# Kernel optimization log

Hardware: AMD Instinct MI355X
Metric: run time of the kernel (lower is better)

The kernel has to match this reference:

```python
import jax, jax.numpy as jnp
import numpy as np

EMBED = 2048
HEADS = 16
DFF = 4 * EMBED
EPS = 1e-5


def layernorm(x, g, b):
    mu = jnp.mean(x, axis=-1, keepdims=True)
    var = jnp.var(x, axis=-1, keepdims=True)
    return (x - mu) * jax.lax.rsqrt(var + EPS) * g + b


def setup_inputs() -> dict:
    key = jax.random.key(0)
    ks = jax.random.split(key, 16)
    s = 1.0 / np.sqrt(EMBED)
    sf = 1.0 / np.sqrt(DFF)
    return {
        "x": jax.random.normal(ks[0], (2, 2048, EMBED), jnp.float32),
        "Wq": jax.random.normal(ks[1], (EMBED, EMBED), jnp.float32) * s,
        "bq": jnp.zeros((EMBED,), jnp.float32),
        "Wk": jax.random.normal(ks[2], (EMBED, EMBED), jnp.float32) * s,
        "bk": jnp.zeros((EMBED,), jnp.float32),
        "Wv": jax.random.normal(ks[3], (EMBED, EMBED), jnp.float32) * s,
        "bv": jnp.zeros((EMBED,), jnp.float32),
        "Wo": jax.random.normal(ks[4], (EMBED, EMBED), jnp.float32) * s,
        "bo": jnp.zeros((EMBED,), jnp.float32),
        "g1": jnp.ones((EMBED,), jnp.float32),
        "b1": jnp.zeros((EMBED,), jnp.float32),
        "g2": jnp.ones((EMBED,), jnp.float32),
        "b2": jnp.zeros((EMBED,), jnp.float32),
        "W1": jax.random.normal(ks[5], (EMBED, DFF), jnp.float32) * s,
        "bf1": jnp.zeros((DFF,), jnp.float32),
        "W2": jax.random.normal(ks[6], (DFF, EMBED), jnp.float32) * sf,
        "bf2": jnp.zeros((EMBED,), jnp.float32),
    }


def reference(x, Wq, bq, Wk, bk, Wv, bv, Wo, bo, g1, b1, g2, b2, W1, bf1, W2, bf2):
    B, N, C = x.shape
    H = HEADS
    hd = C // H
    # QKV projections -> [B, H, N, hd]
    def split_heads(t):
        return t.reshape(B, N, H, hd).transpose(0, 2, 1, 3)
    q = split_heads(x @ Wq + bq)
    k = split_heads(x @ Wk + bk)
    v = split_heads(x @ Wv + bv)
    # scores [B, H, N, N]
    attn = jnp.einsum('bhqd,bhkd->bhqk', q, k) / np.sqrt(hd)
    attn = jax.nn.softmax(attn, axis=-1)
    out = jnp.einsum('bhqk,bhkd->bhqd', attn, v)
    out = out.transpose(0, 2, 1, 3).reshape(B, N, C)
    out = out @ Wo + bo
    h = layernorm(x + out, g1, b1)
    ff = jax.nn.gelu(h @ W1 + bf1, approximate=False) @ W2 + bf2
    return layernorm(h + ff, g2, b2)
```

## Files before the change

kernel.cpp:

```cpp
#include <hip/hip_runtime.h>
#include <math.h>

#define EMBED 2048
#define DFF   8192
#define TOK   4096
#define SEQ   2048
#define HEADS 16
#define HD    128
#define LDQ   6144

typedef __attribute__((ext_vector_type(8))) short short8;
typedef __attribute__((ext_vector_type(4))) float f32x4;

__device__ __forceinline__ unsigned short f2bf(float f) {
    unsigned int u = __float_as_uint(f);
    return (unsigned short)((u + 0x7FFFu + ((u >> 16) & 1u)) >> 16);
}
__device__ __forceinline__ float bf2f(unsigned short s) {
    return __uint_as_float(((unsigned int)s) << 16);
}

__device__ __forceinline__ void async16(const void* g, void* l) {
    __builtin_amdgcn_global_load_lds((const __attribute__((address_space(1))) void*)g,
                                     (__attribute__((address_space(3))) void*)l, 16, 0, 0);
}

__device__ __forceinline__ float gelu_fast(float v) {
    const float y = 1.5957691216057308f * (v + 0.044715f * v * v * v);
    return v / (1.0f + __expf(-y));
}

template<int MODE>
__global__ __launch_bounds__(256, 2)
void gemm_bf16(const unsigned short* __restrict__ A, const unsigned short* __restrict__ B,
               const float* __restrict__ bias, const void* __restrict__ resid,
               unsigned short* __restrict__ C, int M, int N, int K, int lda)
{
    __shared__ __align__(16) float smemf[8448];
    unsigned short* As = (unsigned short*)smemf;
    unsigned short* Bs = As + 8192;
    float* Cs = smemf;

    const int t = threadIdx.x;
    const int w = t >> 6, l = t & 63;
    const int quad = l >> 4, m16 = l & 15;
    const long bm = (long)blockIdx.y * 128, bn = (long)blockIdx.x * 128;
    const int wr = (w >> 1)*64, wc = (w & 1)*64;

    f32x4 acc[4][4] = {};

    const int srow = w*16 + (l >> 2);
    const int sslot = l & 3;
    const unsigned short* Ag = A + (size_t)bm*lda;
    const unsigned short* Bg = B + (size_t)bn*K;

#pragma unroll
    for (int u = 0; u < 2; ++u) {
        const int row = u*64 + srow;
        const int c = sslot ^ ((row >> 1) & 3);
        async16(Ag + (size_t)row*lda + c*8, &As[u*2048 + w*512]);
        async16(Bg + (size_t)row*K   + c*8, &Bs[u*2048 + w*512]);
    }

    const int iters = K >> 5;
    for (int it = 0; it < iters; ++it) {
        __syncthreads();
        if (it + 1 < iters) {
            const int k0 = (it + 1) << 5;
            const int bo = ((it + 1) & 1) * 4096;
#pragma unroll
            for (int u = 0; u < 2; ++u) {
                const int row = u*64 + srow;
                const int c = sslot ^ ((row >> 1) & 3);
                async16(Ag + (size_t)row*lda + k0 + c*8, &As[bo + u*2048 + w*512]);
                async16(Bg + (size_t)row*K   + k0 + c*8, &Bs[bo + u*2048 + w*512]);
            }
        }
        const int co = (it & 1) * 4096;
        short8 af[4], bf[4];
#pragma unroll
        for (int s = 0; s < 4; ++s) {
            const int ra = wr + s*16 + m16;
            const int sla = quad ^ ((ra >> 1) & 3);
            af[s] = *(const short8*)&As[co + ra*32 + sla*8];
            const int rb = wc + s*16 + m16;
            const int slb = quad ^ ((rb >> 1) & 3);
            bf[s] = *(const short8*)&Bs[co + rb*32 + slb*8];
        }
#pragma unroll
        for (int ms = 0; ms < 4; ++ms)
#pragma unroll
            for (int ns = 0; ns < 4; ++ns)
                acc[ms][ns] = __builtin_amdgcn_mfma_f32_16x16x32_bf16(af[ms], bf[ns], acc[ms][ns], 0, 0, 0);
    }

    const int ecol = (t & 15) * 8;
    float bias8[8];
#pragma unroll
    for (int i = 0; i < 8; ++i) bias8[i] = bias[bn + ecol + i];

#pragma unroll
    for (int pass = 0; pass < 2; ++pass) {
        __syncthreads();
        if ((w >> 1) == pass) {
#pragma unroll
            for (int ms = 0; ms < 4; ++ms)
#pragma unroll
                for (int ns = 0; ns < 4; ++ns)
#pragma unroll
                    for (int r = 0; r < 4; ++r)
                        Cs[(ms*16 + quad*4 + r)*132 + wc + ns*16 + m16] = acc[ms][ns][r];
        }
        __syncthreads();
#pragma unroll
        for (int j = 0; j < 4; ++j) {
            const int row = j*16 + (t >> 4);
            float v[8];
            *(f32x4*)&v[0] = *(const f32x4*)&Cs[row*132 + ecol];
            *(f32x4*)&v[4] = *(const f32x4*)&Cs[row*132 + ecol + 4];
            const long gr = bm + pass*64 + row;
            const long go = gr*N + bn + ecol;
            float r8[8];
            if (MODE == 1) {
                *(f32x4*)&r8[0] = *(const f32x4*)((const float*)resid + go);
                *(f32x4*)&r8[4] = *(const f32x4*)((const float*)resid + go + 4);
            }
            short8 rb16;
            if (MODE == 3) rb16 = *(const short8*)((const unsigned short*)resid + go);
            short8 o;
#pragma unroll
            for (int i = 0; i < 8; ++i) {
                float y = v[i] + bias8[i];
                if (MODE == 1) y += r8[i];
                if (MODE == 3) y += bf2f((unsigned short)rb16[i]);
                if (MODE == 2) y = gelu_fast(y);
                o[i] = (short)f2bf(y);
            }
            *(short8*)&C[go] = o;
        }
    }
}

__global__ __launch_bounds__(256, 2)
void attn_flash(unsigned short* __restrict__ qkv)
{
    __shared__ unsigned short Qs[64*128];
    __shared__ unsigned short Ks[64*128];
    __shared__ unsigned short Vt[128*72];
    __shared__ unsigned short Ps[4*16*72];

    const int t = threadIdx.x;
    const int w = t >> 6, l = t & 63;
    const int quad = l >> 4, m16 = l & 15;

    const int qt = blockIdx.x & 31;
    const int bh = blockIdx.x >> 5;
    const int b = bh >> 4, h = bh & 15;

    const long rowq = (long)b*SEQ + qt*64;
    const int qc = h*HD;
    const int kc = EMBED + h*HD;
    const int vc = 2*EMBED + h*HD;

    {
        const int rbase = w*4 + (l >> 4);
        const int slot = l & 15;
#pragma unroll
        for (int u = 0; u < 4; ++u) {
            const int row = u*16 + rbase;
            const int c = slot ^ ((row >> 1) & 7);
            async16(qkv + (rowq + row)*LDQ + qc + c*8, Qs + u*2048 + w*512);
        }
    }
    __syncthreads();

    short8 af[4];
#pragma unroll
    for (int ks = 0; ks < 4; ++ks) {
        const int row = w*16 + m16;
        const int sl = (4*ks + quad) ^ ((row >> 1) & 7);
        af[ks] = *(const short8*)&Qs[row*128 + sl*8];
    }

    f32x4 O[8] = {};
    float mrun[4] = {-1e30f,-1e30f,-1e30f,-1e30f};
    float lrun[4] = {0.f,0.f,0.f,0.f};
    unsigned short* Pw = Ps + w*16*72;

    for (int kt = 0; kt < SEQ/64; ++kt) {
        const long rowkv = (long)b*SEQ + kt*64;
        __syncthreads();
        {
            const int rbase = w*4 + (l >> 4);
            const int slot = l & 15;
#pragma unroll
            for (int u = 0; u < 4; ++u) {
                const int row = u*16 + rbase;
                const int c = slot ^ ((row >> 1) & 7);
                async16(qkv + (rowkv + row)*LDQ + kc + c*8, &Ks[u*2048 + w*512]);
            }
        }
        {
            const int slot = t & 15;
#pragma unroll
            for (int u = 0; u < 2; ++u) {
                const int rp = u*16 + (t >> 4);
                const short8 va = *(const short8*)(qkv + (rowkv + 2*rp    )*LDQ + vc + slot*8);
                const short8 vb = *(const short8*)(qkv + (rowkv + 2*rp + 1)*LDQ + vc + slot*8);
#pragma unroll
                for (int i = 0; i < 8; ++i) {
                    const int d = slot*8 + i;
                    const int col = (2*rp) ^ (((d >> 5) & 3) << 3);
                    unsigned int pv = (unsigned int)(unsigned short)va[i] |
                                      ((unsigned int)(unsigned short)vb[i] << 16);
                    *(unsigned int*)&Vt[d*72 + col] = pv;
                }
            }
        }
        __syncthreads();

        f32x4 S[4];
#pragma unroll
        for (int ns = 0; ns < 4; ++ns) {
            f32x4 a = {0.f,0.f,0.f,0.f};
            const int row = ns*16 + m16;
            const int swr = (row >> 1) & 7;
#pragma unroll
            for (int ks = 0; ks < 4; ++ks) {
                const int sl = (4*ks + quad) ^ swr;
                const short8 bfr = *(const short8*)&Ks[row*128 + sl*8];
                a = __builtin_amdgcn_mfma_f32_16x16x32_bf16(af[ks], bfr, a, 0, 0, 0);
            }
#pragma unroll
            for (int r = 0; r < 4; ++r) a[r] *= 0.08838834764831845f;
            S[ns] = a;
        }

        float al[4], rs[4];
#pragma unroll
        for (int r = 0; r < 4; ++r) {
            float tm = fmaxf(fmaxf(S[0][r], S[1][r]), fmaxf(S[2][r], S[3][r]));
            tm = fmaxf(tm, __shfl_xor(tm, 1));
            tm = fmaxf(tm, __shfl_xor(tm, 2));
            tm = fmaxf(tm, __shfl_xor(tm, 4));
            tm = fmaxf(tm, __shfl_xor(tm, 8));
            const float mn = fmaxf(mrun[r], tm);
            al[r] = __expf(mrun[r] - mn);
            mrun[r] = mn;
            rs[r] = 0.f;
        }
#pragma unroll
        for (int ns = 0; ns < 4; ++ns)
#pragma unroll
            for (int r = 0; r < 4; ++r) {
                const float p = __expf(S[ns][r] - mrun[r]);
                rs[r] += p;
                Pw[(quad*4 + r)*72 + ns*16 + m16] = f2bf(p);
            }
#pragma unroll
        for (int r = 0; r < 4; ++r) {
            rs[r] += __shfl_xor(rs[r], 1);
            rs[r] += __shfl_xor(rs[r], 2);
            rs[r] += __shfl_xor(rs[r], 4);
            rs[r] += __shfl_xor(rs[r], 8);
            lrun[r] = lrun[r]*al[r] + rs[r];
        }
#pragma unroll
        for (int i = 0; i < 8; ++i)
#pragma unroll
            for (int r = 0; r < 4; ++r) O[i][r] *= al[r];

#pragma unroll
        for (int ks2 = 0; ks2 < 2; ++ks2) {
            const short8 ap = *(const short8*)&Pw[m16*72 + ks2*32 + quad*8];
#pragma unroll
            for (int ds = 0; ds < 8; ++ds) {
                const int d = ds*16 + m16;
                const int jcol = (ks2*32 + quad*8) ^ (((d >> 5) & 3) << 3);
                const short8 bv = *(const short8*)&Vt[d*72 + jcol];
                O[ds] = __builtin_amdgcn_mfma_f32_16x16x32_bf16(ap, bv, O[ds], 0, 0, 0);
            }
        }
    }

    float inv[4];
#pragma unroll
    for (int r = 0; r < 4; ++r) inv[r] = 1.0f / lrun[r];
#pragma unroll
    for (int ds = 0; ds < 8; ++ds)
#pragma unroll
        for (int r = 0; r < 4; ++r) {
            const long row = rowq + w*16 + quad*4 + r;
            qkv[row*LDQ + qc + ds*16 + m16] = f2bf(O[ds][r] * inv[r]);
        }
}

template<int OUTF32>
__global__ __launch_bounds__(256)
void ln_bf16(const unsigned short* __restrict__ X, const float* __restrict__ g,
             const float* __restrict__ be, void* __restrict__ Y)
{
    __shared__ float r1[256], r2[256];
    const int t = threadIdx.x;
    const long row = blockIdx.x;
    const unsigned short* x = X + row*EMBED;
    float v[8];
    const short8 xv = *(const short8*)(x + t*8);
    float s = 0.f, s2 = 0.f;
#pragma unroll
    for (int i = 0; i < 8; ++i) {
        v[i] = bf2f((unsigned short)xv[i]);
        s += v[i]; s2 += v[i]*v[i];
    }
    r1[t] = s; r2[t] = s2;
    __syncthreads();
    for (int k = 128; k > 0; k >>= 1) {
        if (t < k) { r1[t] += r1[t+k]; r2[t] += r2[t+k]; }
        __syncthreads();
    }
    const float mu = r1[0] * (1.0f/EMBED);
    const float var = r2[0] * (1.0f/EMBED) - mu*mu;
    const float rstd = rsqrtf(var + 1e-5f);
    if (OUTF32) {
        float* y = (float*)Y + row*EMBED + t*8;
#pragma unroll
        for (int i = 0; i < 8; ++i) y[i] = (v[i]-mu)*rstd*g[t*8+i] + be[t*8+i];
    } else {
        unsigned short* y = (unsigned short*)Y + row*EMBED;
        short8 o;
#pragma unroll
        for (int i = 0; i < 8; ++i) o[i] = (short)f2bf((v[i]-mu)*rstd*g[t*8+i] + be[t*8+i]);
        *(short8*)(y + t*8) = o;
    }
}

__global__ __launch_bounds__(256)
void cvt_transpose(const float* __restrict__ W, unsigned short* __restrict__ Wt, int K, int N)
{
    __shared__ unsigned short T[32][33];
    const int t = threadIdx.x;
    const long n0 = (long)blockIdx.x*32, k0 = (long)blockIdx.y*32;
    {
        const int r = t >> 3, c = (t & 7)*4;
        const float4 vv = *(const float4*)&W[(k0 + r)*N + n0 + c];
        T[r][c+0] = f2bf(vv.x); T[r][c+1] = f2bf(vv.y);
        T[r][c+2] = f2bf(vv.z); T[r][c+3] = f2bf(vv.w);
    }
    __syncthreads();
    const int rn = t >> 3, kk = (t & 7)*4;
    unsigned int p0 = (unsigned int)T[kk+0][rn] | ((unsigned int)T[kk+1][rn] << 16);
    unsigned int p1 = (unsigned int)T[kk+2][rn] | ((unsigned int)T[kk+3][rn] << 16);
    unsigned int* dst = (unsigned int*)&Wt[(n0 + rn)*K + k0 + kk];
    dst[0] = p0; dst[1] = p1;
}

__global__ __launch_bounds__(256)
void cvt_f32_bf16(const float* __restrict__ X, unsigned short* __restrict__ Y, long n)
{
    const long i = ((long)blockIdx.x*256 + threadIdx.x)*8;
    if (i >= n) return;
    const float4 a = *(const float4*)&X[i];
    const float4 b = *(const float4*)&X[i+4];
    short8 o;
    o[0]=(short)f2bf(a.x); o[1]=(short)f2bf(a.y); o[2]=(short)f2bf(a.z); o[3]=(short)f2bf(a.w);
    o[4]=(short)f2bf(b.x); o[5]=(short)f2bf(b.y); o[6]=(short)f2bf(b.z); o[7]=(short)f2bf(b.w);
    *(short8*)&Y[i] = o;
}

__global__ __launch_bounds__(256)
void concat_bias(const float* __restrict__ bq, const float* __restrict__ bk,
                 const float* __restrict__ bv, float* __restrict__ out)
{
    const int i = blockIdx.x*256 + threadIdx.x;
    if (i < 2048) out[i] = bq[i];
    else if (i < 4096) out[i] = bk[i-2048];
    else if (i < 6144) out[i] = bv[i-4096];
}

extern "C" void kernel_launch(void* const* d_in, const int* in_sizes, int n_in,
                              void* d_out, int out_size, void* d_ws, size_t ws_size,
                              hipStream_t stream)
{
    const float* x   = (const float*)d_in[0];
    const float* Wq  = (const float*)d_in[1];
    const float* bq  = (const float*)d_in[2];
    const float* Wk  = (const float*)d_in[3];
    const float* bk  = (const float*)d_in[4];
    const float* Wv  = (const float*)d_in[5];
    const float* bv  = (const float*)d_in[6];
    const float* Wo  = (const float*)d_in[7];
    const float* bo  = (const float*)d_in[8];
    const float* g1  = (const float*)d_in[9];
    const float* b1  = (const float*)d_in[10];
    const float* g2v = (const float*)d_in[11];
    const float* b2v = (const float*)d_in[12];
    const float* W1  = (const float*)d_in[13];
    const float* bf1 = (const float*)d_in[14];
    const float* W2  = (const float*)d_in[15];
    const float* bf2 = (const float*)d_in[16];
    float* out = (float*)d_out;

    char* ws = (char*)d_ws;
    unsigned short* Wqkvt = (unsigned short*)(ws + 0);
    unsigned short* Wot   = (unsigned short*)(ws + 25165824);
    unsigned short* W1t   = (unsigned short*)(ws + 33554432);
    unsigned short* W2t   = (unsigned short*)(ws + 67108864);
    float*          bqkv  = (float*)         (ws + 100663296);
    char* arenaA = ws + 100687872;
    unsigned short* xb   = (unsigned short*)(arenaA);
    unsigned short* qkv  = (unsigned short*)(arenaA + 16777216);
    unsigned short* res1 = (unsigned short*)(arenaA);
    unsigned short* ff   = (unsigned short*)(arenaA);
    unsigned short* hb   = (unsigned short*)(ws + 167796736);
    unsigned short* res2 = (unsigned short*)(ws + 0);

    const dim3 blk(256);

    cvt_transpose<<<dim3(64,64),  blk, 0, stream>>>(Wq, Wqkvt,             2048, 2048);
    cvt_transpose<<<dim3(64,64),  blk, 0, stream>>>(Wk, Wqkvt + 2048*2048, 2048, 2048);
    cvt_transpose<<<dim3(64,64),  blk, 0, stream>>>(Wv, Wqkvt + 2*2048*2048, 2048, 2048);
    cvt_transpose<<<dim3(64,64),  blk, 0, stream>>>(Wo, Wot, 2048, 2048);
    cvt_transpose<<<dim3(256,64), blk, 0, stream>>>(W1, W1t, 2048, 8192);
    cvt_transpose<<<dim3(64,256), blk, 0, stream>>>(W2, W2t, 8192, 2048);
    concat_bias<<<dim3(24), blk, 0, stream>>>(bq, bk, bv, bqkv);
    cvt_f32_bf16<<<dim3(4096), blk, 0, stream>>>(x, xb, (long)TOK*EMBED);

    gemm_bf16<0><<<dim3(48,32), blk, 0, stream>>>(xb, Wqkvt, bqkv, nullptr, qkv, TOK, 6144, 2048, 2048);
    attn_flash<<<dim3(1024), blk, 0, stream>>>(qkv);
    gemm_bf16<1><<<dim3(16,32), blk, 0, stream>>>(qkv, Wot, bo, x, res1, TOK, 2048, 2048, 6144);
    ln_bf16<0><<<dim3(4096), blk, 0, stream>>>(res1, g1, b1, hb);
    gemm_bf16<2><<<dim3(64,32), blk, 0, stream>>>(hb, W1t, bf1, nullptr, ff, TOK, 8192, 2048, 2048);
    gemm_bf16<3><<<dim3(16,32), blk, 0, stream>>>(ff, W2t, bf2, hb, res2, TOK, 2048, 8192, 8192);
    ln_bf16<1><<<dim3(4096), blk, 0, stream>>>(res2, g2v, b2v, out);
}
```

Before: 1.015 ms.

## Double-buffer K tiles and prefetch V into registers in flash attention

Turns the attention K/V loading into a software pipeline. K tiles are double-buffered in LDS, reusing the old Q buffer as the second slot. The next V tile is loaded into registers during the current tile's compute and transposed into LDS after the PV MFMAs, so global latency overlaps with QK^T and softmax work. It also skips rescaling the O accumulator when no running max changed in the wavefront. The cost is more registers under launch_bounds(256,2), plus a barrier around the V transpose.

```diff
diff --git a/kernel.cpp b/kernel.cpp
--- a/kernel.cpp
+++ b/kernel.cpp
@@ -144,8 +144,7 @@
 __global__ __launch_bounds__(256, 2)
 void attn_flash(unsigned short* __restrict__ qkv)
 {
-    __shared__ unsigned short Qs[64*128];
-    __shared__ unsigned short Ks[64*128];
+    __shared__ unsigned short Ks2[2][64*128];
     __shared__ unsigned short Vt[128*72];
     __shared__ unsigned short Ps[4*16*72];
 
@@ -158,18 +157,42 @@
     const int b = bh >> 4, h = bh & 15;
 
     const long rowq = (long)b*SEQ + qt*64;
+    const long rowb = (long)b*SEQ;
     const int qc = h*HD;
     const int kc = EMBED + h*HD;
     const int vc = 2*EMBED + h*HD;
 
-    {
-        const int rbase = w*4 + (l >> 4);
-        const int slot = l & 15;
-#pragma unroll
-        for (int u = 0; u < 4; ++u) {
-            const int row = u*16 + rbase;
-            const int c = slot ^ ((row >> 1) & 7);
-            async16(qkv + (rowq + row)*LDQ + qc + c*8, Qs + u*2048 + w*512);
+    const int rbase = w*4 + (l >> 4);
+    const int slot  = l & 15;
+    const int vslot = t & 15;
+    const int vrp   = t >> 4;
+
+    unsigned short* Qs = Ks2[1];
+
+    short8 va[2], vb[2];
+#pragma unroll
+    for (int u = 0; u < 2; ++u) {
+        const int rp = u*16 + vrp;
+        va[u] = *(const short8*)(qkv + (rowb + 2*rp    )*LDQ + vc + vslot*8);
+        vb[u] = *(const short8*)(qkv + (rowb + 2*rp + 1)*LDQ + vc + vslot*8);
+    }
+#pragma unroll
+    for (int u = 0; u < 4; ++u) {
+        const int row = u*16 + rbase;
+        const int c = slot ^ ((row >> 1) & 7);
+        async16(qkv + (rowq + row)*LDQ + qc + c*8, Qs + u*2048 + w*512);
+        async16(qkv + (rowb + row)*LDQ + kc + c*8, &Ks2[0][u*2048 + w*512]);
+    }
+#pragma unroll
+    for (int u = 0; u < 2; ++u) {
+        const int rp = u*16 + vrp;
+#pragma unroll
+        for (int i = 0; i < 8; ++i) {
+            const int d = vslot*8 + i;
+            const int col = (2*rp) ^ (((d >> 5) & 3) << 3);
+            unsigned int pv = (unsigned int)(unsigned short)va[u][i] |
+                              ((unsigned int)(unsigned short)vb[u][i] << 16);
+            *(unsigned int*)&Vt[d*72 + col] = pv;
         }
     }
     __syncthreads();
@@ -181,6 +204,7 @@
         const int sl = (4*ks + quad) ^ ((row >> 1) & 7);
         af[ks] = *(const short8*)&Qs[row*128 + sl*8];
     }
+    __syncthreads();
 
     f32x4 O[8] = {};
     float mrun[4] = {-1e30f,-1e30f,-1e30f,-1e30f};
@@ -188,36 +212,24 @@
     unsigned short* Pw = Ps + w*16*72;
 
     for (int kt = 0; kt < SEQ/64; ++kt) {
-        const long rowkv = (long)b*SEQ + kt*64;
-        __syncthreads();
-        {
-            const int rbase = w*4 + (l >> 4);
-            const int slot = l & 15;
+        const int cur = kt & 1;
+        const bool pre = (kt + 1 < SEQ/64);
+        const long rowkv = rowb + (long)(kt + 1)*64;
+
+        if (pre) {
+#pragma unroll
+            for (int u = 0; u < 2; ++u) {
+                const int rp = u*16 + vrp;
+                va[u] = *(const short8*)(qkv + (rowkv + 2*rp    )*LDQ + vc + vslot*8);
+                vb[u] = *(const short8*)(qkv + (rowkv + 2*rp + 1)*LDQ + vc + vslot*8);
+            }
 #pragma unroll
             for (int u = 0; u < 4; ++u) {
                 const int row = u*16 + rbase;
                 const int c = slot ^ ((row >> 1) & 7);
-                async16(qkv + (rowkv + row)*LDQ + kc + c*8, &Ks[u*2048 + w*512]);
-            }
-        }
-        {
-            const int slot = t & 15;
-#pragma unroll
-            for (int u = 0; u < 2; ++u) {
-                const int rp = u*16 + (t >> 4);
-                const short8 va = *(const short8*)(qkv + (rowkv + 2*rp    )*LDQ + vc + slot*8);
-                const short8 vb = *(const short8*)(qkv + (rowkv + 2*rp + 1)*LDQ + vc + slot*8);
-#pragma unroll
-                for (int i = 0; i < 8; ++i) {
-                    const int d = slot*8 + i;
-                    const int col = (2*rp) ^ (((d >> 5) & 3) << 3);
-                    unsigned int pv = (unsigned int)(unsigned short)va[i] |
-                                      ((unsigned int)(unsigned short)vb[i] << 16);
-                    *(unsigned int*)&Vt[d*72 + col] = pv;
-                }
-            }
-        }
-        __syncthreads();
+                async16(qkv + (rowkv + row)*LDQ + kc + c*8, &Ks2[cur^1][u*2048 + w*512]);
+            }
+        }
 
         f32x4 S[4];
 #pragma unroll
@@ -228,7 +240,7 @@
 #pragma unroll
             for (int ks = 0; ks < 4; ++ks) {
                 const int sl = (4*ks + quad) ^ swr;
-                const short8 bfr = *(const short8*)&Ks[row*128 + sl*8];
+                const short8 bfr = *(const short8*)&Ks2[cur][row*128 + sl*8];
                 a = __builtin_amdgcn_mfma_f32_16x16x32_bf16(af[ks], bfr, a, 0, 0, 0);
             }
 #pragma unroll
@@ -265,10 +277,12 @@
             rs[r] += __shfl_xor(rs[r], 8);
             lrun[r] = lrun[r]*al[r] + rs[r];
         }
-#pragma unroll
-        for (int i = 0; i < 8; ++i)
-#pragma unroll
-            for (int r = 0; r < 4; ++r) O[i][r] *= al[r];
+        if (__any((al[0] != 1.f) | (al[1] != 1.f) | (al[2] != 1.f) | (al[3] != 1.f))) {
+#pragma unroll
+            for (int i = 0; i < 8; ++i)
+#pragma unroll
+                for (int r = 0; r < 4; ++r) O[i][r] *= al[r];
+        }
 
 #pragma unroll
         for (int ks2 = 0; ks2 < 2; ++ks2) {
@@ -281,6 +295,23 @@
                 O[ds] = __builtin_amdgcn_mfma_f32_16x16x32_bf16(ap, bv, O[ds], 0, 0, 0);
             }
         }
+
+        __syncthreads();
+        if (pre) {
+#pragma unroll
+            for (int u = 0; u < 2; ++u) {
+                const int rp = u*16 + vrp;
+#pragma unroll
+                for (int i = 0; i < 8; ++i) {
+                    const int d = vslot*8 + i;
+                    const int col = (2*rp) ^ (((d >> 5) & 3) << 3);
+                    unsigned int pv = (unsigned int)(unsigned short)va[u][i] |
+                                      ((unsigned int)(unsigned short)vb[u][i] << 16);
+                    *(unsigned int*)&Vt[d*72 + col] = pv;
+                }
+            }
+        }
+        __syncthreads();
     }
 
     float inv[4];
```

Result: faster. 968.7 us (-4.6%).
